# Optimization experiments

Hardware: AMD Instinct MI355X
Metric: run time of the kernel (lower is better)

## Reference

```python
import jax, jax.numpy as jnp
import numpy as np

N = 50000   # nodes
E = 640000  # edges (avg out-degree ~13)
H = 128     # hidden_size
NEG_SLOPE = 0.01  # nn.LeakyReLU default


def setup_inputs() -> dict:
    key = jax.random.key(0)
    k1, k2, k3, k4, k5, k6 = jax.random.split(key, 6)
    node_embeddings = jax.random.normal(k1, (N, H), dtype=jnp.float32)
    edge_embeddings = jax.random.normal(k2, (E, H), dtype=jnp.float32)
    start_nodes = jnp.sort(jax.random.randint(k3, (E,), 0, N, dtype=jnp.int32))
    end_nodes = jax.random.randint(k4, (E,), 0, N, dtype=jnp.int32)
    W1 = jax.random.normal(k5, (H, H), dtype=jnp.float32) / np.sqrt(H)
    W2 = jax.random.normal(k6, (3 * H,), dtype=jnp.float32) / np.sqrt(3 * H)
    return {
        "node_embeddings": node_embeddings,
        "edge_embeddings": edge_embeddings,
        "start_nodes": start_nodes,
        "end_nodes": end_nodes,
        "W1": W1,
        "W2": W2,
    }


def reference(node_embeddings, edge_embeddings, start_nodes, end_nodes, W1, W2):
    # messages = linear_1(node_embeddings)
    messages = node_embeddings @ W1.T                     # [N, H]
    m_i = messages[start_nodes]                           # [E, H] gather src
    m_j = messages[end_nodes]                             # [E, H] gather dst
    # linear_2 on concat([m_i, m_j, e_ij]) == sum of three partial dots
    logits = m_i @ W2[:H] + m_j @ W2[H:2 * H] + edge_embeddings @ W2[2 * H:]
    logits = jnp.where(logits >= 0, logits, NEG_SLOPE * logits)  # leaky_relu
    # segment softmax over edges grouped by start node
    seg_max = jax.ops.segment_max(logits, start_nodes, num_segments=N)  # [N]
    ex = jnp.exp(logits - seg_max[start_nodes])           # [E]
    denom = jax.ops.segment_sum(ex, start_nodes, num_segments=N)        # [N]
    attn = ex / denom[start_nodes]                        # [E]
    # weighted scatter-sum of destination messages back to start nodes
    out = jax.ops.segment_sum(attn[:, None] * m_j, start_nodes, num_segments=N)
    return out  # [N, H]
```

## Files before the change

### kernel.cpp

```cpp
#include <hip/hip_runtime.h>
#include <hip/hip_bf16.h>
#include <cstdint>

#define HDIM 128
#define NEG_SLOPE 0.01f

__device__ __forceinline__ float bf2f(unsigned short u) {
    return __uint_as_float(((uint32_t)u) << 16);
}
__device__ __forceinline__ unsigned short f2bf(float f) {
    __hip_bfloat16 b = __float2bfloat16(f);
    return *reinterpret_cast<unsigned short*>(&b);
}

__global__ __launch_bounds__(256)
void k0_rowptr(const int* __restrict__ start, int* __restrict__ row_ptr,
               int N, int E) {
    int e = blockIdx.x * 256 + threadIdx.x;
    if (e >= E) return;
    int s = start[e];
    if (e == 0) {
        for (int n = 0; n <= s; ++n) row_ptr[n] = 0;
    }
    int snext = (e + 1 < E) ? start[e + 1] : N;
    for (int n = s + 1; n <= snext; ++n) row_ptr[n] = e + 1;
}

#define K1_ROWS 64

__global__ __launch_bounds__(256, 2)
void k1_messages(const float* __restrict__ A, const float* __restrict__ W1,
                 const float* __restrict__ W2, unsigned short* __restrict__ msgb,
                 float* __restrict__ a_src, float* __restrict__ a_dst, int N) {
    __shared__ float W1s[HDIM * HDIM];
    __shared__ float red_a[64 * 17];
    __shared__ float red_b[64 * 17];

    const int tid  = threadIdx.x;
    const int row0 = blockIdx.x * K1_ROWS;

    for (int i = tid; i < HDIM * HDIM / 4; i += 256) {
        int h = i >> 5;
        int g = i & 31;
        float4 v = reinterpret_cast<const float4*>(W1)[i];
        int gs = g ^ ((h >> 3) & 3);
        *reinterpret_cast<float4*>(&W1s[h * HDIM + gs * 4]) = v;
    }
    __syncthreads();

    const int row_t = tid & 15;
    const int col_t = tid >> 4;
    const int h0 = col_t * 8;
    const int sxor = col_t & 3;
    const int wbase = h0 * HDIM;

    int gr[4];
#pragma unroll
    for (int r = 0; r < 4; ++r) {
        int g = row0 + row_t + 16 * r;
        gr[r] = (g < N) ? g : (N - 1);
    }

    float acc[4][8];
#pragma unroll
    for (int r = 0; r < 4; ++r)
#pragma unroll
        for (int c = 0; c < 8; ++c) acc[r][c] = 0.f;

#pragma unroll 2
    for (int k0 = 0; k0 < HDIM; k0 += 4) {
        const int kk = (((k0 >> 2) ^ sxor) << 2);
        float4 a[4];
#pragma unroll
        for (int r = 0; r < 4; ++r)
            a[r] = *reinterpret_cast<const float4*>(&A[(size_t)gr[r] * HDIM + k0]);
#pragma unroll
        for (int c = 0; c < 8; ++c) {
            float4 w = *reinterpret_cast<const float4*>(&W1s[wbase + c * HDIM + kk]);
#pragma unroll
            for (int r = 0; r < 4; ++r) {
                acc[r][c] += a[r].x * w.x + a[r].y * w.y + a[r].z * w.z + a[r].w * w.w;
            }
        }
    }

    float pa[4], pb[4];
#pragma unroll
    for (int r = 0; r < 4; ++r) { pa[r] = 0.f; pb[r] = 0.f; }
#pragma unroll
    for (int c = 0; c < 8; ++c) {
        float wa = W2[h0 + c];
        float wb = W2[HDIM + h0 + c];
#pragma unroll
        for (int r = 0; r < 4; ++r) {
            pa[r] += acc[r][c] * wa;
            pb[r] += acc[r][c] * wb;
        }
    }

#pragma unroll
    for (int r = 0; r < 4; ++r) {
        int g = row0 + row_t + 16 * r;
        if (g < N) {
            uint4 pk;
            pk.x = (uint32_t)f2bf(acc[r][0]) | ((uint32_t)f2bf(acc[r][1]) << 16);
            pk.y = (uint32_t)f2bf(acc[r][2]) | ((uint32_t)f2bf(acc[r][3]) << 16);
            pk.z = (uint32_t)f2bf(acc[r][4]) | ((uint32_t)f2bf(acc[r][5]) << 16);
            pk.w = (uint32_t)f2bf(acc[r][6]) | ((uint32_t)f2bf(acc[r][7]) << 16);
            *reinterpret_cast<uint4*>(&msgb[(size_t)g * HDIM + h0]) = pk;
        }
        red_a[(row_t + 16 * r) * 17 + col_t] = pa[r];
        red_b[(row_t + 16 * r) * 17 + col_t] = pb[r];
    }
    __syncthreads();

    if (tid < K1_ROWS) {
        int g = row0 + tid;
        if (g < N) {
            float sa = 0.f, sb = 0.f;
#pragma unroll
            for (int j = 0; j < 16; ++j) {
                sa += red_a[tid * 17 + j];
                sb += red_b[tid * 17 + j];
            }
            a_src[g] = sa;
            a_dst[g] = sb;
        }
    }
}

__global__ __launch_bounds__(256)
void k23_fused(const float* __restrict__ edge_emb, const float* __restrict__ W2,
               const int* __restrict__ row_ptr, const int* __restrict__ end,
               const float* __restrict__ a_src, const float* __restrict__ a_dst,
               const unsigned short* __restrict__ msgb, float* __restrict__ out,
               int N) {
    const int wid  = threadIdx.x >> 6;
    const int lane = threadIdx.x & 63;
    const int half = lane >> 5;
    const int l32  = lane & 31;
    const int n = blockIdx.x * 4 + wid;
    if (n >= N) return;

    const int lo = row_ptr[n];
    const int hi = row_ptr[n + 1];

    if (lo >= hi) {
        if (half == 0)
            *reinterpret_cast<float4*>(&out[(size_t)n * HDIM + l32 * 4]) =
                make_float4(0.f, 0.f, 0.f, 0.f);
        return;
    }

    const float4 wc = reinterpret_cast<const float4*>(W2 + 2 * HDIM)[l32];
    const float asrc = a_src[n];

    float m = -3.0e38f;
    float s = 0.f;
    float4 acc = make_float4(0.f, 0.f, 0.f, 0.f);

    for (int e = lo + half; e < hi; e += 2) {
        float4 ev = reinterpret_cast<const float4*>(edge_emb)[(size_t)e * 32 + l32];
        int d = end[e];
        float p = ev.x * wc.x + ev.y * wc.y + ev.z * wc.z + ev.w * wc.w;
#pragma unroll
        for (int k = 1; k <= 16; k <<= 1) p += __shfl_xor(p, k);
        float l = p + asrc + a_dst[d];
        l = (l >= 0.f) ? l : NEG_SLOPE * l;
        ushort4 mu = reinterpret_cast<const ushort4*>(msgb)[(size_t)d * 32 + l32];
        float mn = fmaxf(m, l);
        float sc = __expf(m - mn);
        float w  = __expf(l - mn);
        s = s * sc + w;
        acc.x = acc.x * sc + w * bf2f(mu.x);
        acc.y = acc.y * sc + w * bf2f(mu.y);
        acc.z = acc.z * sc + w * bf2f(mu.z);
        acc.w = acc.w * sc + w * bf2f(mu.w);
        m = mn;
    }

    float mo = __shfl_xor(m, 32);
    float so = __shfl_xor(s, 32);
    float4 ao;
    ao.x = __shfl_xor(acc.x, 32);
    ao.y = __shfl_xor(acc.y, 32);
    ao.z = __shfl_xor(acc.z, 32);
    ao.w = __shfl_xor(acc.w, 32);
    float mm = fmaxf(m, mo);
    float e0 = __expf(m - mm);
    float e1 = __expf(mo - mm);
    float inv = 1.f / (s * e0 + so * e1);
    if (half == 0) {
        float4 r;
        r.x = (acc.x * e0 + ao.x * e1) * inv;
        r.y = (acc.y * e0 + ao.y * e1) * inv;
        r.z = (acc.z * e0 + ao.z * e1) * inv;
        r.w = (acc.w * e0 + ao.w * e1) * inv;
        *reinterpret_cast<float4*>(&out[(size_t)n * HDIM + l32 * 4]) = r;
    }
}

extern "C" void kernel_launch(void* const* d_in, const int* in_sizes, int n_in,
                              void* d_out, int out_size, void* d_ws, size_t ws_size,
                              hipStream_t stream) {
    const float* node_emb = (const float*)d_in[0];
    const float* edge_emb = (const float*)d_in[1];
    const int*   start    = (const int*)d_in[2];
    const int*   end      = (const int*)d_in[3];
    const float* W1       = (const float*)d_in[4];
    const float* W2       = (const float*)d_in[5];
    float* out = (float*)d_out;

    const int N = in_sizes[0] / HDIM;
    const int E = in_sizes[2];

    uint8_t* ws = (uint8_t*)d_ws;
    size_t off = 0;
    auto alloc = [&](size_t bytes) {
        void* p = ws + off;
        off = (off + bytes + 511) & ~(size_t)511;
        return p;
    };
    unsigned short* msgb = (unsigned short*)alloc((size_t)N * HDIM * sizeof(unsigned short));
    float* a_src   = (float*)alloc((size_t)N * sizeof(float));
    float* a_dst   = (float*)alloc((size_t)N * sizeof(float));
    int*   row_ptr = (int*)alloc((size_t)(N + 1) * sizeof(int));

    k0_rowptr<<<(E + 255) / 256, 256, 0, stream>>>(start, row_ptr, N, E);
    k1_messages<<<(N + K1_ROWS - 1) / K1_ROWS, 256, 0, stream>>>(
        node_emb, W1, W2, msgb, a_src, a_dst, N);
    k23_fused<<<(N + 3) / 4, 256, 0, stream>>>(edge_emb, W2, row_ptr, end,
                                               a_src, a_dst, msgb, out, N);
}
```

Baseline: 163.0 us.

## Co-schedule edge logit streaming with message GEMM and batch aggregation over edges

Moves the edge_emb·W2c dot product out of the aggregation kernel into extra blocks of the GEMM launch, interleaving GEMM blocks with streaming blocks so the bandwidth-bound edge pass runs alongside the compute-bound W1 GEMM. The aggregation kernel now reads a precomputed per-edge scalar and processes edges in batches of 8 with a full 64-lane wave over 2 bf16 features per lane. This removes the half-wave split and its cross-half merge. The cost is an extra E-float workspace round trip, and the streaming blocks now request the larger shared-memory allocation even though they only use W2c, which may reduce occupancy.

```diff
diff --git a/kernel.cpp b/kernel.cpp
--- a/kernel.cpp
+++ b/kernel.cpp
@@ -5,9 +5,6 @@
 #define HDIM 128
 #define NEG_SLOPE 0.01f
 
-__device__ __forceinline__ float bf2f(unsigned short u) {
-    return __uint_as_float(((uint32_t)u) << 16);
-}
 __device__ __forceinline__ unsigned short f2bf(float f) {
     __hip_bfloat16 b = __float2bfloat16(f);
     return *reinterpret_cast<unsigned short*>(&b);
@@ -29,15 +26,56 @@
 #define K1_ROWS 64
 
 __global__ __launch_bounds__(256, 2)
-void k1_messages(const float* __restrict__ A, const float* __restrict__ W1,
-                 const float* __restrict__ W2, unsigned short* __restrict__ msgb,
-                 float* __restrict__ a_src, float* __restrict__ a_dst, int N) {
-    __shared__ float W1s[HDIM * HDIM];
-    __shared__ float red_a[64 * 17];
-    __shared__ float red_b[64 * 17];
-
-    const int tid  = threadIdx.x;
-    const int row0 = blockIdx.x * K1_ROWS;
+void k12_parallel(const float* __restrict__ A, const float* __restrict__ W1,
+                  const float* __restrict__ W2, unsigned short* __restrict__ msgb,
+                  float* __restrict__ a_src, float* __restrict__ a_dst, int N,
+                  const float* __restrict__ edge_emb, float* __restrict__ praw,
+                  int E, int Gg, int interleave) {
+    __shared__ float smem[HDIM * HDIM + 2 * 64 * 17];
+
+    const int bid = blockIdx.x;
+    const int tid = threadIdx.x;
+
+    int gemm_id = -1, stream_id = 0;
+    if (interleave) {
+        if (bid < 4 * Gg) {
+            if ((bid & 3) == 0) gemm_id = bid >> 2;
+            else stream_id = (bid >> 2) * 3 + (bid & 3) - 1;
+        } else {
+            stream_id = 3 * Gg + (bid - 4 * Gg);
+        }
+    } else {
+        if (bid < Gg) gemm_id = bid;
+        else stream_id = bid - Gg;
+    }
+
+    if (gemm_id < 0) {
+        float* w2s = smem;
+        if (tid < 32)
+            *reinterpret_cast<float4*>(&w2s[tid * 4]) =
+                reinterpret_cast<const float4*>(W2 + 2 * HDIM)[tid];
+        __syncthreads();
+
+        int e = stream_id * 256 + tid;
+        if (e < E) {
+            const float4* row = reinterpret_cast<const float4*>(edge_emb) + (size_t)e * 32;
+            float p = 0.f;
+#pragma unroll 8
+            for (int g = 0; g < 32; ++g) {
+                float4 ev = row[g];
+                float4 w  = *reinterpret_cast<const float4*>(&w2s[g * 4]);
+                p += ev.x * w.x + ev.y * w.y + ev.z * w.z + ev.w * w.w;
+            }
+            praw[e] = p;
+        }
+        return;
+    }
+
+    float* W1s   = smem;
+    float* red_a = smem + HDIM * HDIM;
+    float* red_b = red_a + 64 * 17;
+
+    const int row0 = gemm_id * K1_ROWS;
 
     for (int i = tid; i < HDIM * HDIM / 4; i += 256) {
         int h = i >> 5;
@@ -129,16 +167,16 @@
     }
 }
 
+#define KB 8
+
 __global__ __launch_bounds__(256)
-void k23_fused(const float* __restrict__ edge_emb, const float* __restrict__ W2,
-               const int* __restrict__ row_ptr, const int* __restrict__ end,
-               const float* __restrict__ a_src, const float* __restrict__ a_dst,
-               const unsigned short* __restrict__ msgb, float* __restrict__ out,
-               int N) {
+void k3_aggregate(const float* __restrict__ praw, const int* __restrict__ row_ptr,
+                  const int* __restrict__ end, const float* __restrict__ a_src,
+                  const float* __restrict__ a_dst,
+                  const unsigned short* __restrict__ msgb,
+                  float* __restrict__ out, int N) {
     const int wid  = threadIdx.x >> 6;
     const int lane = threadIdx.x & 63;
-    const int half = lane >> 5;
-    const int l32  = lane & 31;
     const int n = blockIdx.x * 4 + wid;
     if (n >= N) return;
 
@@ -146,58 +184,59 @@
     const int hi = row_ptr[n + 1];
 
     if (lo >= hi) {
-        if (half == 0)
-            *reinterpret_cast<float4*>(&out[(size_t)n * HDIM + l32 * 4]) =
-                make_float4(0.f, 0.f, 0.f, 0.f);
+        *reinterpret_cast<float2*>(&out[(size_t)n * HDIM + lane * 2]) =
+            make_float2(0.f, 0.f);
         return;
     }
 
-    const float4 wc = reinterpret_cast<const float4*>(W2 + 2 * HDIM)[l32];
     const float asrc = a_src[n];
-
     float m = -3.0e38f;
     float s = 0.f;
-    float4 acc = make_float4(0.f, 0.f, 0.f, 0.f);
-
-    for (int e = lo + half; e < hi; e += 2) {
-        float4 ev = reinterpret_cast<const float4*>(edge_emb)[(size_t)e * 32 + l32];
-        int d = end[e];
-        float p = ev.x * wc.x + ev.y * wc.y + ev.z * wc.z + ev.w * wc.w;
-#pragma unroll
-        for (int k = 1; k <= 16; k <<= 1) p += __shfl_xor(p, k);
-        float l = p + asrc + a_dst[d];
-        l = (l >= 0.f) ? l : NEG_SLOPE * l;
-        ushort4 mu = reinterpret_cast<const ushort4*>(msgb)[(size_t)d * 32 + l32];
-        float mn = fmaxf(m, l);
+    float2 acc = make_float2(0.f, 0.f);
+
+    for (int base = lo; base < hi; base += KB) {
+        float lv[KB];
+        uint32_t mu[KB];
+        const int cnt = hi - base;
+
+#pragma unroll
+        for (int i = 0; i < KB; ++i) {
+            if (i < cnt) {
+                int e = base + i;
+                int d = end[e];
+                mu[i] = reinterpret_cast<const uint32_t*>(msgb)[(size_t)d * 64 + lane];
+                float l = praw[e] + asrc + a_dst[d];
+                lv[i] = (l >= 0.f) ? l : NEG_SLOPE * l;
+            } else {
+                mu[i] = 0;
+                lv[i] = -3.0e38f;
+            }
+        }
+
+        float bm = lv[0];
+#pragma unroll
+        for (int i = 1; i < KB; ++i) bm = fmaxf(bm, lv[i]);
+        float mn = fmaxf(m, bm);
         float sc = __expf(m - mn);
-        float w  = __expf(l - mn);
-        s = s * sc + w;
-        acc.x = acc.x * sc + w * bf2f(mu.x);
-        acc.y = acc.y * sc + w * bf2f(mu.y);
-        acc.z = acc.z * sc + w * bf2f(mu.z);
-        acc.w = acc.w * sc + w * bf2f(mu.w);
+
+        float bs = 0.f;
+        float2 ba = make_float2(0.f, 0.f);
+#pragma unroll
+        for (int i = 0; i < KB; ++i) {
+            float w = __expf(lv[i] - mn);
+            bs += w;
+            ba.x += w * __uint_as_float(mu[i] << 16);
+            ba.y += w * __uint_as_float(mu[i] & 0xffff0000u);
+        }
+        s = s * sc + bs;
+        acc.x = acc.x * sc + ba.x;
+        acc.y = acc.y * sc + ba.y;
         m = mn;
     }
 
-    float mo = __shfl_xor(m, 32);
-    float so = __shfl_xor(s, 32);
-    float4 ao;
-    ao.x = __shfl_xor(acc.x, 32);
-    ao.y = __shfl_xor(acc.y, 32);
-    ao.z = __shfl_xor(acc.z, 32);
-    ao.w = __shfl_xor(acc.w, 32);
-    float mm = fmaxf(m, mo);
-    float e0 = __expf(m - mm);
-    float e1 = __expf(mo - mm);
-    float inv = 1.f / (s * e0 + so * e1);
-    if (half == 0) {
-        float4 r;
-        r.x = (acc.x * e0 + ao.x * e1) * inv;
-        r.y = (acc.y * e0 + ao.y * e1) * inv;
-        r.z = (acc.z * e0 + ao.z * e1) * inv;
-        r.w = (acc.w * e0 + ao.w * e1) * inv;
-        *reinterpret_cast<float4*>(&out[(size_t)n * HDIM + l32 * 4]) = r;
-    }
+    const float inv = 1.f / s;
+    *reinterpret_cast<float2*>(&out[(size_t)n * HDIM + lane * 2]) =
+        make_float2(acc.x * inv, acc.y * inv);
 }
 
 extern "C" void kernel_launch(void* const* d_in, const int* in_sizes, int n_in,
@@ -224,11 +263,17 @@
     unsigned short* msgb = (unsigned short*)alloc((size_t)N * HDIM * sizeof(unsigned short));
     float* a_src   = (float*)alloc((size_t)N * sizeof(float));
     float* a_dst   = (float*)alloc((size_t)N * sizeof(float));
+    float* praw    = (float*)alloc((size_t)E * sizeof(float));
     int*   row_ptr = (int*)alloc((size_t)(N + 1) * sizeof(int));
 
+    const int Gg = (N + K1_ROWS - 1) / K1_ROWS;
+    const int Gs = (E + 255) / 256;
+    const int interleave = (Gs >= 3 * Gg) ? 1 : 0;
+
     k0_rowptr<<<(E + 255) / 256, 256, 0, stream>>>(start, row_ptr, N, E);
-    k1_messages<<<(N + K1_ROWS - 1) / K1_ROWS, 256, 0, stream>>>(
-        node_emb, W1, W2, msgb, a_src, a_dst, N);
-    k23_fused<<<(N + 3) / 4, 256, 0, stream>>>(edge_emb, W2, row_ptr, end,
-                                               a_src, a_dst, msgb, out, N);
-}
+    k12_parallel<<<Gg + Gs, 256, 0, stream>>>(node_emb, W1, W2, msgb, a_src,
+                                              a_dst, N, edge_emb, praw, E, Gg,
+                                              interleave);
+    k3_aggregate<<<(N + 3) / 4, 256, 0, stream>>>(praw, row_ptr, end, a_src,
+                                                  a_dst, msgb, out, N);
+}
```

After: 289.7 us. 1.78x slower.
